# Optimization experiments

Measured on AMD Instinct MI355X. Metric: run time of the kernel, lower is better.

Reference implementation:

```python
import itertools
import jax, jax.numpy as jnp
import numpy as np

B = 4096        # n_cases
N_IN = 6        # input variables
N_MF = 4        # MFs per variable
N_OUT = 1
N_RULES = N_MF ** N_IN  # 4096 (itertools.product of MF indices)


def setup_inputs() -> dict:
    key = jax.random.key(0)
    kx, kc = jax.random.split(key, 2)
    x = jax.random.normal(kx, (B, N_IN), dtype=jnp.float32)
    # Bell MF params per (variable, mf): half-width a, slope b, center c
    a = jnp.ones((N_IN, N_MF), dtype=jnp.float32)
    b = jnp.full((N_IN, N_MF), 2.0, dtype=jnp.float32)
    c = jnp.tile(jnp.linspace(-2.0, 2.0, N_MF, dtype=jnp.float32), (N_IN, 1))
    # TSK consequent coefficients: [n_rules, n_out, n_in+1]
    coeff = jax.random.normal(kc, (N_RULES, N_OUT, N_IN + 1), dtype=jnp.float32) * 0.1
    # all combinations of MF indices, one row per rule: [n_rules, n_in]
    mf_indices = jnp.asarray(
        np.array(list(itertools.product(*[range(N_MF)] * N_IN)), dtype=np.int32))
    return {"x": x, "a": a, "b": b, "c": c, "coeff": coeff,
            "mf_indices": mf_indices}


def reference(x, a, b, c, coeff, mf_indices):
    # Fuzzify: generalized bell MF, 1 / (1 + ((x-c)/a)^2)^b  -> [B, n_in, n_mf]
    dist = ((x[:, :, None] - c) / a) ** 2
    memb = 1.0 / (1.0 + dist ** b)
    # Antecedent: gather each rule's MF value per variable -> [B, n_rules, n_in]
    var_ids = jnp.arange(memb.shape[1])[None, :]          # [1, n_in]
    ants = memb[:, var_ids, mf_indices]                    # [B, n_rules, n_in]
    rules = jnp.prod(ants, axis=2)                         # [B, n_rules]
    # L1-normalize fire strengths (F.normalize p=1)
    weights = rules / jnp.clip(jnp.sum(rules, axis=1, keepdims=True), 1e-12)
    # TSK consequent: coeff @ [x; 1] -> [B, n_out, n_rules]
    x_plus = jnp.concatenate([x, jnp.ones((x.shape[0], 1), x.dtype)], axis=1)
    tsk = jnp.einsum('roi,bi->bor', coeff, x_plus)
    # Weighted combine -> [B, n_out]
    return jnp.einsum('bor,br->bo', tsk, weights)
```

## Files before the change

kernel.cpp:

```cpp
#include <hip/hip_runtime.h>

#define NI 6
#define NM 4
#define NC 7
#define NRULES 4096
#define ROWS_PER_BLOCK 16
#define RULES_PER_TILE 1024
#define RH_PER_TILE 16

__global__ __launch_bounds__(256, 4)
void anfis_main(const float* __restrict__ x, const float* __restrict__ a,
                const float* __restrict__ b, const float* __restrict__ c,
                const float* __restrict__ coeff, float* __restrict__ ws) {
    __shared__ float sCT[NC][RULES_PER_TILE];
    __shared__ float sMemb[ROWS_PER_BLOCK][NI][NM];
    __shared__ float sPhi[ROWS_PER_BLOCK][RH_PER_TILE];
    __shared__ float sPlo[ROWS_PER_BLOCK][64];

    const int tid = threadIdx.x;
    const int bx = blockIdx.x;
    const int ruleTile = bx & 3;
    const int rowTile  = bx >> 2;
    const int row0 = rowTile * ROWS_PER_BLOCK;
    const int ruleBase = ruleTile * RULES_PER_TILE;

    for (int idx = tid; idx < RULES_PER_TILE * NC; idx += 256) {
        int rr = idx / NC;
        int i  = idx - rr * NC;
        sCT[i][rr] = coeff[(size_t)(ruleBase + rr) * NC + i];
    }

    for (int idx = tid; idx < ROWS_PER_BLOCK * NI * NM; idx += 256) {
        int row = idx / (NI * NM);
        int rem = idx - row * (NI * NM);
        int j = rem >> 2;
        int k = rem & 3;
        float xv = x[(row0 + row) * NI + j];
        float av = a[j * NM + k];
        float bv = b[j * NM + k];
        float cv = c[j * NM + k];
        float t = (xv - cv) / av;
        float dist = t * t;
        float db = powf(dist, bv);
        sMemb[row][j][k] = 1.0f / (1.0f + db);
    }
    __syncthreads();

    if (tid < ROWS_PER_BLOCK * RH_PER_TILE) {
        int row = tid >> 4;
        int rhl = tid & 15;
        int rh = ruleTile * RH_PER_TILE + rhl;
        sPhi[row][rhl] = sMemb[row][0][(rh >> 4) & 3] *
                         sMemb[row][1][(rh >> 2) & 3] *
                         sMemb[row][2][rh & 3];
    }
    for (int idx = tid; idx < ROWS_PER_BLOCK * 64; idx += 256) {
        int row = idx >> 6;
        int t64 = idx & 63;
        sPlo[row][t64] = sMemb[row][3][(t64 >> 4) & 3] *
                         sMemb[row][4][(t64 >> 2) & 3] *
                         sMemb[row][5][t64 & 3];
    }
    __syncthreads();

    const int wave = tid >> 6;
    const int lane = tid & 63;
    const int lw0 = wave * 4;

    float plo[4];
    float acc[4][8];
    #pragma unroll
    for (int r = 0; r < 4; ++r) {
        plo[r] = sPlo[lw0 + r][lane];
        #pragma unroll
        for (int i = 0; i < 8; ++i) acc[r][i] = 0.0f;
    }

    #pragma unroll 4
    for (int rhl = 0; rhl < RH_PER_TILE; ++rhl) {
        float cv[NC];
        #pragma unroll
        for (int i = 0; i < NC; ++i) cv[i] = sCT[i][rhl * 64 + lane];
        #pragma unroll
        for (int r = 0; r < 4; ++r) {
            float w = sPhi[lw0 + r][rhl] * plo[r];
            acc[r][7] += w;
            #pragma unroll
            for (int i = 0; i < NC; ++i)
                acc[r][i] = fmaf(w, cv[i], acc[r][i]);
        }
    }

    #pragma unroll
    for (int r = 0; r < 4; ++r) {
        #pragma unroll
        for (int i = 0; i < 8; ++i) {
            float v = acc[r][i];
            #pragma unroll
            for (int s = 1; s < 64; s <<= 1) v += __shfl_xor(v, s, 64);
            acc[r][i] = v;
        }
    }

    if (lane == 0) {
        #pragma unroll
        for (int r = 0; r < 4; ++r) {
            int row = row0 + lw0 + r;
            #pragma unroll
            for (int i = 0; i < 8; ++i)
                atomicAdd(&ws[row * 8 + i], acc[r][i]);
        }
    }
}

__global__ __launch_bounds__(256)
void anfis_finalize(const float* __restrict__ ws, const float* __restrict__ x,
                    float* __restrict__ out, int B) {
    int row = blockIdx.x * blockDim.x + threadIdx.x;
    if (row >= B) return;
    float num = ws[row * 8 + 6];
    #pragma unroll
    for (int j = 0; j < NI; ++j)
        num = fmaf(ws[row * 8 + j], x[row * NI + j], num);
    float den = ws[row * 8 + 7];
    out[row] = num / fmaxf(den, 1e-12f);
}

extern "C" void kernel_launch(void* const* d_in, const int* in_sizes, int n_in,
                              void* d_out, int out_size, void* d_ws, size_t ws_size,
                              hipStream_t stream) {
    const float* x     = (const float*)d_in[0];
    const float* a     = (const float*)d_in[1];
    const float* b     = (const float*)d_in[2];
    const float* c     = (const float*)d_in[3];
    const float* coeff = (const float*)d_in[4];
    float* out = (float*)d_out;
    float* ws  = (float*)d_ws;

    const int B = in_sizes[0] / NI;

    hipMemsetAsync(ws, 0, (size_t)B * 8 * sizeof(float), stream);

    const int rowTiles = B / ROWS_PER_BLOCK;
    anfis_main<<<dim3(rowTiles * 4), dim3(256), 0, stream>>>(x, a, b, c, coeff, ws);
    anfis_finalize<<<dim3((B + 255) / 256), dim3(256), 0, stream>>>(ws, x, out, B);
}
```

Baseline: 82.87 us.

## Fuse ANFIS main and finalize into one kernel covering all rules per block

Each block now handles all 4096 rules for its 16 rows, using 512 threads in two wave halves that each take half the rules. The coefficients are staged through shared memory in two passes, and the two halves are combined through a shared-memory reduction. This removes the memset, the global atomics and the separate finalize launch, with the output computed directly. In exchange each block loads the whole coefficient table (112 KB), there are four times fewer blocks with twice the threads, and an extra pass with syncs is added.

```diff
diff --git a/kernel.cpp b/kernel.cpp
--- a/kernel.cpp
+++ b/kernel.cpp
@@ -3,96 +3,92 @@
 #define NI 6
 #define NM 4
 #define NC 7
-#define NRULES 4096
 #define ROWS_PER_BLOCK 16
-#define RULES_PER_TILE 1024
-#define RH_PER_TILE 16
+#define RPW 4
 
-__global__ __launch_bounds__(256, 4)
-void anfis_main(const float* __restrict__ x, const float* __restrict__ a,
-                const float* __restrict__ b, const float* __restrict__ c,
-                const float* __restrict__ coeff, float* __restrict__ ws) {
-    __shared__ float sCT[NC][RULES_PER_TILE];
+__global__ __launch_bounds__(512, 2)
+void anfis_fused(const float* __restrict__ x, const float* __restrict__ a,
+                 const float* __restrict__ b, const float* __restrict__ c,
+                 const float* __restrict__ coeff, float* __restrict__ out) {
+    __shared__ float sCT[2][NC][1024];
     __shared__ float sMemb[ROWS_PER_BLOCK][NI][NM];
-    __shared__ float sPhi[ROWS_PER_BLOCK][RH_PER_TILE];
-    __shared__ float sPlo[ROWS_PER_BLOCK][64];
+    __shared__ float sPhi[ROWS_PER_BLOCK][64];
+    __shared__ float sRed[4][RPW][8];
 
-    const int tid = threadIdx.x;
-    const int bx = blockIdx.x;
-    const int ruleTile = bx & 3;
-    const int rowTile  = bx >> 2;
-    const int row0 = rowTile * ROWS_PER_BLOCK;
-    const int ruleBase = ruleTile * RULES_PER_TILE;
+    const int tid  = threadIdx.x;
+    const int row0 = blockIdx.x * ROWS_PER_BLOCK;
+    const int wave = tid >> 6;
+    const int lane = tid & 63;
+    const int g = wave >> 1;
+    const int h = wave & 1;
 
-    for (int idx = tid; idx < RULES_PER_TILE * NC; idx += 256) {
-        int rr = idx / NC;
-        int i  = idx - rr * NC;
-        sCT[i][rr] = coeff[(size_t)(ruleBase + rr) * NC + i];
-    }
-
-    for (int idx = tid; idx < ROWS_PER_BLOCK * NI * NM; idx += 256) {
-        int row = idx / (NI * NM);
-        int rem = idx - row * (NI * NM);
-        int j = rem >> 2;
-        int k = rem & 3;
+    if (tid < ROWS_PER_BLOCK * NI * NM) {
+        int row = tid / (NI * NM);
+        int rem = tid % (NI * NM);
+        int j = rem >> 2, k = rem & 3;
         float xv = x[(row0 + row) * NI + j];
-        float av = a[j * NM + k];
-        float bv = b[j * NM + k];
-        float cv = c[j * NM + k];
-        float t = (xv - cv) / av;
+        float t = (xv - c[j * NM + k]) / a[j * NM + k];
         float dist = t * t;
-        float db = powf(dist, bv);
-        sMemb[row][j][k] = 1.0f / (1.0f + db);
+        sMemb[row][j][k] = 1.0f / (1.0f + powf(dist, b[j * NM + k]));
     }
     __syncthreads();
 
-    if (tid < ROWS_PER_BLOCK * RH_PER_TILE) {
-        int row = tid >> 4;
-        int rhl = tid & 15;
-        int rh = ruleTile * RH_PER_TILE + rhl;
-        sPhi[row][rhl] = sMemb[row][0][(rh >> 4) & 3] *
-                         sMemb[row][1][(rh >> 2) & 3] *
-                         sMemb[row][2][rh & 3];
+    for (int idx = tid; idx < ROWS_PER_BLOCK * 64; idx += 512) {
+        int row = idx >> 6, rh = idx & 63;
+        sPhi[row][rh] = sMemb[row][0][(rh >> 4) & 3] *
+                        sMemb[row][1][(rh >> 2) & 3] *
+                        sMemb[row][2][rh & 3];
     }
-    for (int idx = tid; idx < ROWS_PER_BLOCK * 64; idx += 256) {
-        int row = idx >> 6;
-        int t64 = idx & 63;
-        sPlo[row][t64] = sMemb[row][3][(t64 >> 4) & 3] *
-                         sMemb[row][4][(t64 >> 2) & 3] *
-                         sMemb[row][5][t64 & 3];
+
+    float plo[RPW];
+    {
+        int d3 = (lane >> 4) & 3, d4 = (lane >> 2) & 3, d5 = lane & 3;
+        #pragma unroll
+        for (int r = 0; r < RPW; ++r) {
+            int row = g * RPW + r;
+            plo[r] = sMemb[row][3][d3] * sMemb[row][4][d4] * sMemb[row][5][d5];
+        }
     }
+
+    float acc[RPW][8];
+    #pragma unroll
+    for (int r = 0; r < RPW; ++r)
+        #pragma unroll
+        for (int i = 0; i < 8; ++i) acc[r][i] = 0.0f;
+
     __syncthreads();
 
-    const int wave = tid >> 6;
-    const int lane = tid & 63;
-    const int lw0 = wave * 4;
+    for (int p = 0; p < 2; ++p) {
+        if (p) __syncthreads();
 
-    float plo[4];
-    float acc[4][8];
-    #pragma unroll
-    for (int r = 0; r < 4; ++r) {
-        plo[r] = sPlo[lw0 + r][lane];
-        #pragma unroll
-        for (int i = 0; i < 8; ++i) acc[r][i] = 0.0f;
-    }
+        for (int idx = tid; idx < 2 * 7168; idx += 512) {
+            int s   = (idx >= 7168) ? 1 : 0;
+            int rem = idx - s * 7168;
+            int rr  = rem / NC;
+            int i   = rem - rr * NC;
+            sCT[s][i][rr] = coeff[idx + (s + p) * 7168];
+        }
+        __syncthreads();
 
-    #pragma unroll 4
-    for (int rhl = 0; rhl < RH_PER_TILE; ++rhl) {
-        float cv[NC];
-        #pragma unroll
-        for (int i = 0; i < NC; ++i) cv[i] = sCT[i][rhl * 64 + lane];
-        #pragma unroll
-        for (int r = 0; r < 4; ++r) {
-            float w = sPhi[lw0 + r][rhl] * plo[r];
-            acc[r][7] += w;
+        #pragma unroll 4
+        for (int rhl = 0; rhl < 16; ++rhl) {
+            const int rh = h * 32 + p * 16 + rhl;
+            float cv[NC];
             #pragma unroll
-            for (int i = 0; i < NC; ++i)
-                acc[r][i] = fmaf(w, cv[i], acc[r][i]);
+            for (int i = 0; i < NC; ++i) cv[i] = sCT[h][i][rhl * 64 + lane];
+            #pragma unroll
+            for (int r = 0; r < RPW; ++r) {
+                float w = sPhi[g * RPW + r][rh] * plo[r];
+                acc[r][7] += w;
+                #pragma unroll
+                for (int i = 0; i < NC; ++i)
+                    acc[r][i] = fmaf(w, cv[i], acc[r][i]);
+            }
         }
     }
 
     #pragma unroll
-    for (int r = 0; r < 4; ++r) {
+    for (int r = 0; r < RPW; ++r)
         #pragma unroll
         for (int i = 0; i < 8; ++i) {
             float v = acc[r][i];
@@ -100,30 +96,26 @@
             for (int s = 1; s < 64; s <<= 1) v += __shfl_xor(v, s, 64);
             acc[r][i] = v;
         }
+
+    if (h == 1 && lane == 0) {
+        #pragma unroll
+        for (int r = 0; r < RPW; ++r)
+            #pragma unroll
+            for (int i = 0; i < 8; ++i) sRed[g][r][i] = acc[r][i];
     }
-
-    if (lane == 0) {
+    __syncthreads();
+    if (h == 0 && lane == 0) {
         #pragma unroll
-        for (int r = 0; r < 4; ++r) {
-            int row = row0 + lw0 + r;
+        for (int r = 0; r < RPW; ++r) {
+            int row = row0 + g * RPW + r;
+            float den = acc[r][7] + sRed[g][r][7];
+            float num = acc[r][6] + sRed[g][r][6];
             #pragma unroll
-            for (int i = 0; i < 8; ++i)
-                atomicAdd(&ws[row * 8 + i], acc[r][i]);
+            for (int j = 0; j < NI; ++j)
+                num = fmaf(acc[r][j] + sRed[g][r][j], x[row * NI + j], num);
+            out[row] = num / fmaxf(den, 1e-12f);
         }
     }
-}
-
-__global__ __launch_bounds__(256)
-void anfis_finalize(const float* __restrict__ ws, const float* __restrict__ x,
-                    float* __restrict__ out, int B) {
-    int row = blockIdx.x * blockDim.x + threadIdx.x;
-    if (row >= B) return;
-    float num = ws[row * 8 + 6];
-    #pragma unroll
-    for (int j = 0; j < NI; ++j)
-        num = fmaf(ws[row * 8 + j], x[row * NI + j], num);
-    float den = ws[row * 8 + 7];
-    out[row] = num / fmaxf(den, 1e-12f);
 }
 
 extern "C" void kernel_launch(void* const* d_in, const int* in_sizes, int n_in,
@@ -135,13 +127,7 @@
     const float* c     = (const float*)d_in[3];
     const float* coeff = (const float*)d_in[4];
     float* out = (float*)d_out;
-    float* ws  = (float*)d_ws;
 
     const int B = in_sizes[0] / NI;
-
-    hipMemsetAsync(ws, 0, (size_t)B * 8 * sizeof(float), stream);
-
-    const int rowTiles = B / ROWS_PER_BLOCK;
-    anfis_main<<<dim3(rowTiles * 4), dim3(256), 0, stream>>>(x, a, b, c, coeff, ws);
-    anfis_finalize<<<dim3((B + 255) / 256), dim3(256), 0, stream>>>(ws, x, out, B);
+    anfis_fused<<<dim3(B / ROWS_PER_BLOCK), dim3(512), 0, stream>>>(x, a, b, c, coeff, out);
 }
```

Result: faster. 78.03 us (-5.8%).
